# Kernel tuning notes

Measured on AMD Instinct MI355X. Metric: run time of the kernel, lower is better.

The kernel has to match this reference:

```python
import jax, jax.numpy as jnp
import numpy as np

B, S, D, T, H = 4, 2048, 1024, 5, 8


def setup_inputs() -> dict:
    key = jax.random.key(0)
    ks = jax.random.split(key, 12)
    sc = 0.02  # small init scale for weights so attention logits stay sane
    return {
        "x": jax.random.normal(ks[0], (B, S, D), jnp.float32),
        "time_steps": jax.random.randint(ks[1], (B, S), 0, T),
        "gamma": jnp.ones((T, D), jnp.float32),
        "beta": jax.random.normal(ks[2], (T, D), jnp.float32) * sc,
        "decay": jnp.ones((T,), jnp.float32),
        "shift_W": jax.random.normal(ks[3], (D, D), jnp.float32) * sc,
        "shift_b": jax.random.normal(ks[4], (D,), jnp.float32) * sc,
        "in_proj_W": jax.random.normal(ks[5], (3 * D, D), jnp.float32) * sc,
        "in_proj_b": jax.random.normal(ks[6], (3 * D,), jnp.float32) * sc,
        "out_proj_W": jax.random.normal(ks[7], (D, D), jnp.float32) * sc,
        "out_proj_b": jax.random.normal(ks[8], (D,), jnp.float32) * sc,
    }


def reference(x, time_steps, gamma, beta, decay, shift_W, shift_b,
              in_proj_W, in_proj_b, out_proj_W, out_proj_b):
    eps = 1e-5
    T_ = gamma.shape[0]
    b_, s_, d_ = x.shape
    hd = d_ // H

    # --- per-token indexed LayerNorm + decay (vectorized gather of norm params) ---
    idx = jnp.clip(time_steps, 0, T_ - 1)              # safe gather index [B,S]
    mu = jnp.mean(x, axis=-1, keepdims=True)
    var = jnp.mean(jnp.square(x - mu), axis=-1, keepdims=True)
    xn = (x - mu) * jax.lax.rsqrt(var + eps)           # [B,S,D]
    normed = (xn * gamma[idx] + beta[idx]) * decay[idx][..., None]
    x = jnp.where((time_steps < T_)[..., None], normed, x)

    # --- residual temporal shift (Linear) ---
    x = x + x @ shift_W.T + shift_b

    # --- torch-style MultiheadAttention(x, x, x), batch_first ---
    qkv = x @ in_proj_W.T + in_proj_b                  # [B,S,3D]
    q, k, v = jnp.split(qkv, 3, axis=-1)
    q = q.reshape(b_, s_, H, hd)
    k = k.reshape(b_, s_, H, hd)
    v = v.reshape(b_, s_, H, hd)
    scale = 1.0 / jnp.sqrt(jnp.asarray(hd, x.dtype))
    scores = jnp.einsum('bqhd,bkhd->bhqk', q, k) * scale   # [B,H,S,S]
    attn = jax.nn.softmax(scores, axis=-1)
    ctx = jnp.einsum('bhqk,bkhd->bqhd', attn, v).reshape(b_, s_, d_)
    attended = ctx @ out_proj_W.T + out_proj_b
    return x + attended
```

## Files before the change

kernel.cpp:

```cpp
#include <hip/hip_runtime.h>
#include <math.h>

#define B_ 4
#define S_ 2048
#define D_ 1024
#define T_ 5
#define H_ 8
#define HD_ 128
#define M_ (B_*S_)

typedef __bf16 bf16x8 __attribute__((ext_vector_type(8)));
typedef float  f32x4  __attribute__((ext_vector_type(4)));

__device__ __forceinline__ float bf2f(unsigned short u) {
    union { unsigned int i; float f; } c; c.i = ((unsigned int)u) << 16; return c.f;
}
__device__ __forceinline__ unsigned short f2bf(float f) {
    union { float f; unsigned int i; } c; c.f = f;
    unsigned int u = c.i;
    u += 0x7fffu + ((u >> 16) & 1u);
    return (unsigned short)(u >> 16);
}

__device__ __forceinline__ void gll16(const void* g, void* l) {
    __builtin_amdgcn_global_load_lds(
        (const __attribute__((address_space(1))) void*)g,
        (__attribute__((address_space(3))) void*)l, 16, 0, 0);
}

__global__ __launch_bounds__(256) void f2bf_kernel(
    const float* __restrict__ src, unsigned short* __restrict__ dst)
{
    int i = (blockIdx.x * 256 + threadIdx.x) * 4;
    float4 v = *(const float4*)(src + i);
    ushort4 o;
    o.x = f2bf(v.x); o.y = f2bf(v.y); o.z = f2bf(v.z); o.w = f2bf(v.w);
    *(ushort4*)(dst + i) = o;
}

__global__ __launch_bounds__(256) void ln_kernel(
    const float* __restrict__ x, const int* __restrict__ ts,
    const float* __restrict__ gamma, const float* __restrict__ beta,
    const float* __restrict__ decay, unsigned short* __restrict__ out)
{
    int row = blockIdx.x;
    int tid = threadIdx.x;
    float4 v = ((const float4*)(x + (size_t)row * D_))[tid];
    float s  = v.x + v.y + v.z + v.w;
    float s2 = v.x*v.x + v.y*v.y + v.z*v.z + v.w*v.w;
    #pragma unroll
    for (int off = 32; off; off >>= 1) {
        s  += __shfl_down(s,  off);
        s2 += __shfl_down(s2, off);
    }
    __shared__ float ps[4], ps2[4];
    if ((tid & 63) == 0) { ps[tid >> 6] = s; ps2[tid >> 6] = s2; }
    __syncthreads();
    float tot  = ps[0]  + ps[1]  + ps[2]  + ps[3];
    float tot2 = ps2[0] + ps2[1] + ps2[2] + ps2[3];
    float mu   = tot  * (1.0f / D_);
    float var  = tot2 * (1.0f / D_) - mu * mu;
    float rstd = rsqrtf(var + 1e-5f);

    int t  = ts[row];
    int tc = min(max(t, 0), T_ - 1);
    float4 g = ((const float4*)(gamma + (size_t)tc * D_))[tid];
    float4 b = ((const float4*)(beta  + (size_t)tc * D_))[tid];
    float dec = decay[tc];

    float4 o;
    o.x = ((v.x - mu) * rstd * g.x + b.x) * dec;
    o.y = ((v.y - mu) * rstd * g.y + b.y) * dec;
    o.z = ((v.z - mu) * rstd * g.z + b.z) * dec;
    o.w = ((v.w - mu) * rstd * g.w + b.w) * dec;
    if (t >= T_) o = v;
    ushort4 ob;
    ob.x = f2bf(o.x); ob.y = f2bf(o.y); ob.z = f2bf(o.z); ob.w = f2bf(o.w);
    ((ushort4*)(out + (size_t)row * D_))[tid] = ob;
}

__global__ __launch_bounds__(256) void gemm_mfma(
    const unsigned short* __restrict__ A,
    const unsigned short* __restrict__ Wt,
    const float* __restrict__ bias,
    const float* __restrict__ ResF,
    const unsigned short* __restrict__ ResB,
    float* __restrict__ Cf,
    unsigned short* __restrict__ Cb,
    int M, int N, int K)
{
    __shared__ __align__(16) unsigned short As[128 * 32];
    __shared__ __align__(16) unsigned short Bs[128 * 32];
    int tid  = threadIdx.x;
    int w    = tid >> 6, lane = tid & 63;
    int lm   = lane & 15, quad = lane >> 4;
    int wm   = w & 1,  wn   = w >> 1;
    int i0 = blockIdx.y * 128, j0 = blockIdx.x * 128;

    f32x4 acc[4][4];
    #pragma unroll
    for (int mt = 0; mt < 4; ++mt)
        #pragma unroll
        for (int nt = 0; nt < 4; ++nt)
            acc[mt][nt] = (f32x4){0.f, 0.f, 0.f, 0.f};

    int c0 = w * 128 + lane;
    int r0 = c0 >> 2,   k80 = (c0 & 3) * 8;
    int c1 = c0 + 64;
    int r1 = c1 >> 2,   k81 = (c1 & 3) * 8;

    for (int kt = 0; kt < K; kt += 32) {
        __syncthreads();
        gll16(A  + (size_t)(i0 + r0) * K + kt + k80, As + (size_t)(w * 128 + 0 ) * 8);
        gll16(A  + (size_t)(i0 + r1) * K + kt + k81, As + (size_t)(w * 128 + 64) * 8);
        gll16(Wt + (size_t)(j0 + r0) * K + kt + k80, Bs + (size_t)(w * 128 + 0 ) * 8);
        gll16(Wt + (size_t)(j0 + r1) * K + kt + k81, Bs + (size_t)(w * 128 + 64) * 8);
        __syncthreads();

        bf16x8 af[4], bfr[4];
        #pragma unroll
        for (int mt = 0; mt < 4; ++mt)
            af[mt] = *(const bf16x8*)&As[(wm * 64 + mt * 16 + lm) * 32 + quad * 8];
        #pragma unroll
        for (int nt = 0; nt < 4; ++nt)
            bfr[nt] = *(const bf16x8*)&Bs[(wn * 64 + nt * 16 + lm) * 32 + quad * 8];
        #pragma unroll
        for (int mt = 0; mt < 4; ++mt)
            #pragma unroll
            for (int nt = 0; nt < 4; ++nt)
                acc[mt][nt] = __builtin_amdgcn_mfma_f32_16x16x32_bf16(
                    af[mt], bfr[nt], acc[mt][nt], 0, 0, 0);
    }

    #pragma unroll
    for (int nt = 0; nt < 4; ++nt) {
        int j = j0 + wn * 64 + nt * 16 + lm;
        float bj = bias[j];
        #pragma unroll
        for (int mt = 0; mt < 4; ++mt) {
            #pragma unroll
            for (int r = 0; r < 4; ++r) {
                int i = i0 + wm * 64 + mt * 16 + quad * 4 + r;
                size_t off = (size_t)i * N + j;
                float v = acc[mt][nt][r] + bj;
                if (ResF) v += ResF[off];
                else if (ResB) v += bf2f(ResB[off]);
                if (Cf) Cf[off] = v;
                if (Cb) Cb[off] = f2bf(v);
            }
        }
    }
}

__global__ __launch_bounds__(256) void transpose_v(
    const unsigned short* __restrict__ qkv, unsigned short* __restrict__ vt)
{
    __shared__ unsigned short Ts[64][72];
    int t = threadIdx.x;
    int s0 = blockIdx.x * 64, c0 = blockIdx.y * 64, b = blockIdx.z;
    int r  = t >> 2, cg = (t & 3) * 16;
    const unsigned short* src =
        qkv + (size_t)(b * S_ + s0 + r) * (3 * D_) + 2 * D_ + c0 + cg;
    *(bf16x8*)&Ts[r][cg]     = *(const bf16x8*)(src);
    *(bf16x8*)&Ts[r][cg + 8] = *(const bf16x8*)(src + 8);
    __syncthreads();
    int dd = t >> 2, sg = (t & 3) * 16;
    unsigned short tmp[16];
    #pragma unroll
    for (int j = 0; j < 16; ++j) tmp[j] = Ts[sg + j][dd];
    unsigned short* dst = vt + ((size_t)b * D_ + c0 + dd) * S_ + s0 + sg;
    *(bf16x8*)dst       = *(bf16x8*)&tmp[0];
    *(bf16x8*)(dst + 8) = *(bf16x8*)&tmp[8];
}

__global__ __launch_bounds__(256, 2) void flash_mfma(
    const unsigned short* __restrict__ qkv,
    const unsigned short* __restrict__ vt,
    unsigned short* __restrict__ ctx)
{
    __shared__ unsigned short Ks [64][136];
    __shared__ unsigned short Vts[128][72];
    __shared__ unsigned short Ps [4][32][72];

    int tid  = threadIdx.x;
    int w    = tid >> 6, lane = tid & 63;
    int lm   = lane & 15, quad = lane >> 4;
    int qt = blockIdx.x, h = blockIdx.y, b = blockIdx.z;
    const int rs = 3 * D_;
    const float scale = 0.08838834764831844f;
    size_t qbase  = (size_t)b * S_ * rs + (size_t)h * HD_;
    size_t kbase  = qbase + D_;
    size_t vtbase = ((size_t)b * H_ + h) * (size_t)HD_ * S_;
    int q0 = qt * 128 + w * 32;

    bf16x8 qf[2][4];
    #pragma unroll
    for (int mt = 0; mt < 2; ++mt)
        #pragma unroll
        for (int kc = 0; kc < 4; ++kc) {
            bf16x8 raw = *(const bf16x8*)(
                qkv + qbase + (size_t)(q0 + mt * 16 + lm) * rs + kc * 32 + quad * 8);
            bf16x8 sc;
            #pragma unroll
            for (int j = 0; j < 8; ++j) {
                unsigned short u;
                __builtin_memcpy(&u, (const char*)&raw + 2 * j, 2);
                u = f2bf(bf2f(u) * scale);
                __builtin_memcpy((char*)&sc + 2 * j, &u, 2);
            }
            qf[mt][kc] = sc;
        }

    f32x4 oacc[2][8];
    #pragma unroll
    for (int mt = 0; mt < 2; ++mt)
        #pragma unroll
        for (int n = 0; n < 8; ++n)
            oacc[mt][n] = (f32x4){0.f, 0.f, 0.f, 0.f};
    float lst[2][4];
    #pragma unroll
    for (int mt = 0; mt < 2; ++mt)
        #pragma unroll
        for (int r = 0; r < 4; ++r) lst[mt][r] = 0.f;

    for (int kt = 0; kt < S_ / 64; ++kt) {
        int k0 = kt * 64;
        __syncthreads();
        #pragma unroll
        for (int i = 0; i < 4; ++i) {
            int chunk = tid + 256 * i;
            int r = chunk >> 4, cc = chunk & 15;
            bf16x8 kv8 = *(const bf16x8*)(
                qkv + kbase + (size_t)(k0 + r) * rs + cc * 8);
            *(bf16x8*)&Ks[r][cc * 8] = kv8;
        }
        #pragma unroll
        for (int i = 0; i < 4; ++i) {
            int chunk = tid + 256 * i;
            int d = chunk >> 3, cc = chunk & 7;
            bf16x8 vv8 = *(const bf16x8*)(
                vt + vtbase + (size_t)d * S_ + k0 + cc * 8);
            *(bf16x8*)&Vts[d][cc * 8] = vv8;
        }
        __syncthreads();

        f32x4 sacc[2][4];
        #pragma unroll
        for (int mt = 0; mt < 2; ++mt)
            #pragma unroll
            for (int n = 0; n < 4; ++n)
                sacc[mt][n] = (f32x4){0.f, 0.f, 0.f, 0.f};
        #pragma unroll
        for (int n = 0; n < 4; ++n) {
            bf16x8 bk[4];
            #pragma unroll
            for (int kc = 0; kc < 4; ++kc)
                bk[kc] = *(const bf16x8*)&Ks[n * 16 + lm][kc * 32 + quad * 8];
            #pragma unroll
            for (int mt = 0; mt < 2; ++mt)
                #pragma unroll
                for (int kc = 0; kc < 4; ++kc)
                    sacc[mt][n] = __builtin_amdgcn_mfma_f32_16x16x32_bf16(
                        qf[mt][kc], bk[kc], sacc[mt][n], 0, 0, 0);
        }

        #pragma unroll
        for (int mt = 0; mt < 2; ++mt) {
            #pragma unroll
            for (int r = 0; r < 4; ++r) {
                float p0 = __expf(sacc[mt][0][r]);
                float p1 = __expf(sacc[mt][1][r]);
                float p2 = __expf(sacc[mt][2][r]);
                float p3 = __expf(sacc[mt][3][r]);
                lst[mt][r] += (p0 + p1) + (p2 + p3);
                int row = mt * 16 + quad * 4 + r;
                Ps[w][row][ 0 + lm] = f2bf(p0);
                Ps[w][row][16 + lm] = f2bf(p1);
                Ps[w][row][32 + lm] = f2bf(p2);
                Ps[w][row][48 + lm] = f2bf(p3);
            }
        }

        bf16x8 pa[2][2];
        #pragma unroll
        for (int mt = 0; mt < 2; ++mt)
            #pragma unroll
            for (int kc = 0; kc < 2; ++kc)
                pa[mt][kc] = *(const bf16x8*)&Ps[w][mt * 16 + lm][kc * 32 + quad * 8];
        #pragma unroll
        for (int n = 0; n < 8; ++n) {
            bf16x8 bv0 = *(const bf16x8*)&Vts[n * 16 + lm][quad * 8];
            bf16x8 bv1 = *(const bf16x8*)&Vts[n * 16 + lm][32 + quad * 8];
            #pragma unroll
            for (int mt = 0; mt < 2; ++mt) {
                oacc[mt][n] = __builtin_amdgcn_mfma_f32_16x16x32_bf16(
                    pa[mt][0], bv0, oacc[mt][n], 0, 0, 0);
                oacc[mt][n] = __builtin_amdgcn_mfma_f32_16x16x32_bf16(
                    pa[mt][1], bv1, oacc[mt][n], 0, 0, 0);
            }
        }
    }

    float linv[2][4];
    #pragma unroll
    for (int mt = 0; mt < 2; ++mt)
        #pragma unroll
        for (int r = 0; r < 4; ++r) {
            float l = lst[mt][r];
            l += __shfl_xor(l, 1);
            l += __shfl_xor(l, 2);
            l += __shfl_xor(l, 4);
            l += __shfl_xor(l, 8);
            linv[mt][r] = 1.0f / l;
        }
    size_t rowbase = (size_t)b * S_ + (size_t)qt * 128 + w * 32;
    #pragma unroll
    for (int mt = 0; mt < 2; ++mt)
        #pragma unroll
        for (int r = 0; r < 4; ++r) {
            size_t row = rowbase + mt * 16 + quad * 4 + r;
            unsigned short* dst = ctx + row * D_ + h * HD_ + lm;
            #pragma unroll
            for (int n = 0; n < 8; ++n)
                dst[n * 16] = f2bf(oacc[mt][n][r] * linv[mt][r]);
        }
}

extern "C" void kernel_launch(void* const* d_in, const int* in_sizes, int n_in,
                              void* d_out, int out_size, void* d_ws, size_t ws_size,
                              hipStream_t stream) {
    (void)in_sizes; (void)n_in; (void)out_size; (void)ws_size;
    const float* x          = (const float*)d_in[0];
    const int*   ts         = (const int*)  d_in[1];
    const float* gamma      = (const float*)d_in[2];
    const float* beta       = (const float*)d_in[3];
    const float* decay      = (const float*)d_in[4];
    const float* shift_W    = (const float*)d_in[5];
    const float* shift_b    = (const float*)d_in[6];
    const float* in_proj_W  = (const float*)d_in[7];
    const float* in_proj_b  = (const float*)d_in[8];
    const float* out_proj_W = (const float*)d_in[9];
    const float* out_proj_b = (const float*)d_in[10];
    float* out = (float*)d_out;

    unsigned short* p     = (unsigned short*)d_ws;
    unsigned short* xln_b = p;
    unsigned short* qkv_b = xln_b + (size_t)M_ * D_;
    unsigned short* xs_b  = qkv_b + (size_t)M_ * 3 * D_;
    unsigned short* wsh_b = xs_b  + (size_t)M_ * D_;
    unsigned short* wip_b = wsh_b + (size_t)D_ * D_;
    unsigned short* wop_b = wip_b + (size_t)3 * D_ * D_;
    unsigned short* vt_b  = xs_b;
    unsigned short* ctx_b = xln_b;
    float* xs = out;

    f2bf_kernel<<<D_ * D_ / 1024,     256, 0, stream>>>(shift_W,    wsh_b);
    f2bf_kernel<<<3 * D_ * D_ / 1024, 256, 0, stream>>>(in_proj_W,  wip_b);
    f2bf_kernel<<<D_ * D_ / 1024,     256, 0, stream>>>(out_proj_W, wop_b);

    ln_kernel<<<M_, 256, 0, stream>>>(x, ts, gamma, beta, decay, xln_b);

    gemm_mfma<<<dim3(D_ / 128, M_ / 128), 256, 0, stream>>>(
        xln_b, wsh_b, shift_b, nullptr, xln_b, xs, xs_b, M_, D_, D_);
    gemm_mfma<<<dim3(3 * D_ / 128, M_ / 128), 256, 0, stream>>>(
        xs_b, wip_b, in_proj_b, nullptr, nullptr, nullptr, qkv_b, M_, 3 * D_, D_);

    transpose_v<<<dim3(S_ / 64, D_ / 64, B_), 256, 0, stream>>>(qkv_b, vt_b);
    flash_mfma<<<dim3(S_ / 128, H_, B_), 256, 0, stream>>>(qkv_b, vt_b, ctx_b);

    gemm_mfma<<<dim3(D_ / 128, M_ / 128), 256, 0, stream>>>(
        ctx_b, wop_b, out_proj_b, xs, nullptr, out, nullptr, M_, D_, D_);
}
```

Measured before the change: 409.5 us.

## Fuse weight conversions, swizzle GEMM block order, use exp2 in attention

Merges the three weight fp32-to-bf16 conversion launches into one kernel that picks its source pointer by index, which relies on the three bf16 weight buffers sitting next to each other in the workspace. The GEMM remaps linear block IDs with a stride-8 swizzle so that neighbouring workgroups work on different row tiles, likely aiming at better L2 reuse across XCDs. Flash attention folds log2(e) into the Q scale and calls exp2f instead of __expf. Together these cut launch overhead and may improve cache locality and the cost of exponentials.

```diff
diff --git a/kernel.cpp b/kernel.cpp
--- a/kernel.cpp
+++ b/kernel.cpp
@@ -28,11 +28,19 @@
         (__attribute__((address_space(3))) void*)l, 16, 0, 0);
 }
 
-__global__ __launch_bounds__(256) void f2bf_kernel(
-    const float* __restrict__ src, unsigned short* __restrict__ dst)
+__global__ __launch_bounds__(256) void f2bf3_kernel(
+    const float* __restrict__ s0,
+    const float* __restrict__ s1,
+    const float* __restrict__ s2,
+    unsigned short* __restrict__ dst)
 {
     int i = (blockIdx.x * 256 + threadIdx.x) * 4;
-    float4 v = *(const float4*)(src + i);
+    const float* src;
+    int local;
+    if (i < D_ * D_)              { src = s0; local = i; }
+    else if (i < 4 * D_ * D_)     { src = s1; local = i - D_ * D_; }
+    else                          { src = s2; local = i - 4 * D_ * D_; }
+    float4 v = *(const float4*)(src + local);
     ushort4 o;
     o.x = f2bf(v.x); o.y = f2bf(v.y); o.z = f2bf(v.z); o.w = f2bf(v.w);
     *(ushort4*)(dst + i) = o;
@@ -95,7 +103,14 @@
     int w    = tid >> 6, lane = tid & 63;
     int lm   = lane & 15, quad = lane >> 4;
     int wm   = w & 1,  wn   = w >> 1;
-    int i0 = blockIdx.y * 128, j0 = blockIdx.x * 128;
+
+    int nwgx  = gridDim.x;
+    int lin   = blockIdx.y * nwgx + blockIdx.x;
+    int chunk = (nwgx * gridDim.y) >> 3;
+    int swz   = (lin & 7) * chunk + (lin >> 3);
+    int bx    = swz % nwgx, by = swz / nwgx;
+
+    int i0 = by * 128, j0 = bx * 128;
 
     f32x4 acc[4][4];
     #pragma unroll
@@ -187,7 +202,7 @@
     int lm   = lane & 15, quad = lane >> 4;
     int qt = blockIdx.x, h = blockIdx.y, b = blockIdx.z;
     const int rs = 3 * D_;
-    const float scale = 0.08838834764831844f;
+    const float scale = 0.08838834764831844f * 1.4426950408889634f;
     size_t qbase  = (size_t)b * S_ * rs + (size_t)h * HD_;
     size_t kbase  = qbase + D_;
     size_t vtbase = ((size_t)b * H_ + h) * (size_t)HD_ * S_;
@@ -268,10 +283,10 @@
         for (int mt = 0; mt < 2; ++mt) {
             #pragma unroll
             for (int r = 0; r < 4; ++r) {
-                float p0 = __expf(sacc[mt][0][r]);
-                float p1 = __expf(sacc[mt][1][r]);
-                float p2 = __expf(sacc[mt][2][r]);
-                float p3 = __expf(sacc[mt][3][r]);
+                float p0 = exp2f(sacc[mt][0][r]);
+                float p1 = exp2f(sacc[mt][1][r]);
+                float p2 = exp2f(sacc[mt][2][r]);
+                float p3 = exp2f(sacc[mt][3][r]);
                 lst[mt][r] += (p0 + p1) + (p2 + p3);
                 int row = mt * 16 + quad * 4 + r;
                 Ps[w][row][ 0 + lm] = f2bf(p0);
@@ -354,9 +369,8 @@
     unsigned short* ctx_b = xln_b;
     float* xs = out;
 
-    f2bf_kernel<<<D_ * D_ / 1024,     256, 0, stream>>>(shift_W,    wsh_b);
-    f2bf_kernel<<<3 * D_ * D_ / 1024, 256, 0, stream>>>(in_proj_W,  wip_b);
-    f2bf_kernel<<<D_ * D_ / 1024,     256, 0, stream>>>(out_proj_W, wop_b);
+    f2bf3_kernel<<<5 * D_ * D_ / 1024, 256, 0, stream>>>(
+        shift_W, in_proj_W, out_proj_W, wsh_b);
 
     ln_kernel<<<M_, 256, 0, stream>>>(x, ts, gamma, beta, decay, xln_b);
 
```

After: 412.3 us. About the same (+0.7%).
